# Kernel tuning notes

Hardware: AMD Instinct MI355X
Metric: run time of the kernel (lower is better)

The kernel has to match this reference:

```python
import jax, jax.numpy as jnp
import numpy as np

NUM_USERS = 1_000_000
NUM_MOVIES = 100_000
EMBED_DIM = 64
MLP_SIZES = [16, 8, 4]
BATCH = 16384


def setup_inputs() -> dict:
    key = jax.random.key(0)
    ks = jax.random.split(key, 12)
    s = 0.05
    inp = {
        "user_ids": jax.random.randint(ks[0], (BATCH,), 0, NUM_USERS, dtype=jnp.int32),
        "movie_ids": jax.random.randint(ks[1], (BATCH,), 0, NUM_MOVIES, dtype=jnp.int32),
        "gmf_user_emb": jax.random.normal(ks[2], (NUM_USERS, EMBED_DIM), jnp.float32) * s,
        "gmf_movie_emb": jax.random.normal(ks[3], (NUM_MOVIES, EMBED_DIM), jnp.float32) * s,
        "mlp_user_emb": jax.random.normal(ks[4], (NUM_USERS, MLP_SIZES[0] // 2), jnp.float32) * s,
        "mlp_movie_emb": jax.random.normal(ks[5], (NUM_MOVIES, MLP_SIZES[0] // 2), jnp.float32) * s,
        "W1": jax.random.normal(ks[6], (MLP_SIZES[0], MLP_SIZES[1]), jnp.float32) * s,
        "b1": jnp.zeros((MLP_SIZES[1],), jnp.float32),
        "W2": jax.random.normal(ks[7], (MLP_SIZES[1], MLP_SIZES[2]), jnp.float32) * s,
        "b2": jnp.zeros((MLP_SIZES[2],), jnp.float32),
        "Wf": jax.random.normal(ks[8], (EMBED_DIM + MLP_SIZES[2], 1), jnp.float32) * s,
        "bf": jnp.zeros((1,), jnp.float32),
    }
    return inp


def reference(user_ids, movie_ids, gmf_user_emb, gmf_movie_emb,
              mlp_user_emb, mlp_movie_emb, W1, b1, W2, b2, Wf, bf):
    # GMF branch: elementwise product of gathered embeddings  [B, E]
    gmf_out = gmf_user_emb[user_ids] * gmf_movie_emb[movie_ids]
    # MLP branch: concat gathered halves -> 16 -> 8 -> 4 with ReLU
    mlp_in = jnp.concatenate([mlp_user_emb[user_ids], mlp_movie_emb[movie_ids]], axis=-1)
    h = jax.nn.relu(mlp_in @ W1 + b1)
    h = jax.nn.relu(h @ W2 + b2)
    combined = jnp.concatenate([gmf_out, h], axis=-1)  # [B, E+4]
    logits = combined @ Wf + bf                        # [B, 1]
    out = jax.nn.sigmoid(logits).squeeze(-1) * 4.0 + 1.0
    return out
```

## Files before the change

kernel.cpp:

```cpp
#include <hip/hip_runtime.h>

#define BATCH 16384

__global__ __launch_bounds__(64) void neumf_kernel(
    const int*   __restrict__ user_ids,
    const int*   __restrict__ movie_ids,
    const float* __restrict__ gmf_user,
    const float* __restrict__ gmf_movie,
    const float* __restrict__ mlp_user,
    const float* __restrict__ mlp_movie,
    const float* __restrict__ W1,
    const float* __restrict__ b1,
    const float* __restrict__ W2,
    const float* __restrict__ b2,
    const float* __restrict__ Wf,
    const float* __restrict__ bf,
    float*       __restrict__ out)
{
    int i = blockIdx.x * blockDim.x + threadIdx.x;
    if (i >= BATCH) return;

    const int uid = user_ids[i];
    const int mid = movie_ids[i];

    const float4* u4 = (const float4*)(gmf_user  + (size_t)uid * 64);
    const float4* m4 = (const float4*)(gmf_movie + (size_t)mid * 64);
    const float4* w4 = (const float4*)Wf;

    float acc = 0.f;
    #pragma unroll
    for (int j = 0; j < 16; ++j) {
        float4 a = u4[j];
        float4 b = m4[j];
        float4 w = w4[j];
        acc += a.x * b.x * w.x;
        acc += a.y * b.y * w.y;
        acc += a.z * b.z * w.z;
        acc += a.w * b.w * w.w;
    }

    float in16[16];
    {
        const float4* mu = (const float4*)(mlp_user  + (size_t)uid * 8);
        const float4* mm = (const float4*)(mlp_movie + (size_t)mid * 8);
        float4 t;
        t = mu[0]; in16[0]  = t.x; in16[1]  = t.y; in16[2]  = t.z; in16[3]  = t.w;
        t = mu[1]; in16[4]  = t.x; in16[5]  = t.y; in16[6]  = t.z; in16[7]  = t.w;
        t = mm[0]; in16[8]  = t.x; in16[9]  = t.y; in16[10] = t.z; in16[11] = t.w;
        t = mm[1]; in16[12] = t.x; in16[13] = t.y; in16[14] = t.z; in16[15] = t.w;
    }

    float h1[8];
    #pragma unroll
    for (int j = 0; j < 8; ++j) {
        float s = b1[j];
        #pragma unroll
        for (int k = 0; k < 16; ++k) s = fmaf(in16[k], W1[k * 8 + j], s);
        h1[j] = fmaxf(s, 0.f);
    }

    #pragma unroll
    for (int j = 0; j < 4; ++j) {
        float s = b2[j];
        #pragma unroll
        for (int k = 0; k < 8; ++k) s = fmaf(h1[k], W2[k * 4 + j], s);
        s = fmaxf(s, 0.f);
        acc = fmaf(s, Wf[64 + j], acc);
    }

    const float logit = acc + bf[0];
    const float sig = 1.f / (1.f + __expf(-logit));
    out[i] = sig * 4.f + 1.f;
}

extern "C" void kernel_launch(void* const* d_in, const int* in_sizes, int n_in,
                              void* d_out, int out_size, void* d_ws, size_t ws_size,
                              hipStream_t stream) {
    const int*   user_ids  = (const int*)  d_in[0];
    const int*   movie_ids = (const int*)  d_in[1];
    const float* gmf_user  = (const float*)d_in[2];
    const float* gmf_movie = (const float*)d_in[3];
    const float* mlp_user  = (const float*)d_in[4];
    const float* mlp_movie = (const float*)d_in[5];
    const float* W1        = (const float*)d_in[6];
    const float* b1        = (const float*)d_in[7];
    const float* W2        = (const float*)d_in[8];
    const float* b2        = (const float*)d_in[9];
    const float* Wf        = (const float*)d_in[10];
    const float* bf        = (const float*)d_in[11];
    float*       out       = (float*)d_out;

    const int threads = 64;
    const int blocks  = (BATCH + threads - 1) / threads;
    neumf_kernel<<<blocks, threads, 0, stream>>>(
        user_ids, movie_ids, gmf_user, gmf_movie, mlp_user, mlp_movie,
        W1, b1, W2, b2, Wf, bf, out);
}
```

Before: 9.705 us.

## Split each batch element across 16 lanes with shuffle reduction

Assigns 16 threads per batch element so each lane loads one float4 of the GMF embeddings, which makes the gathered rows coalesced. Partial dot products are combined with xor shuffles. The MLP inputs are loaded by four lanes and broadcast with shuffles. Every lane then computes the small MLP redundantly and lane 0 writes the output. Block size rises to 256. The aim is better memory coalescing and more parallelism for the random gathers, at the cost of redundant MLP arithmetic and shuffle overhead.

```diff
diff --git a/kernel.cpp b/kernel.cpp
--- a/kernel.cpp
+++ b/kernel.cpp
@@ -1,8 +1,9 @@
 #include <hip/hip_runtime.h>
 
 #define BATCH 16384
+#define SPLIT 16
 
-__global__ __launch_bounds__(64) void neumf_kernel(
+__global__ __launch_bounds__(256) void neumf_kernel(
     const int*   __restrict__ user_ids,
     const int*   __restrict__ movie_ids,
     const float* __restrict__ gmf_user,
@@ -17,37 +18,39 @@
     const float* __restrict__ bf,
     float*       __restrict__ out)
 {
-    int i = blockIdx.x * blockDim.x + threadIdx.x;
-    if (i >= BATCH) return;
+    const int tid   = blockIdx.x * blockDim.x + threadIdx.x;
+    const int elem  = tid >> 4;
+    const int lane  = tid & (SPLIT - 1);
+    if (elem >= BATCH) return;
 
-    const int uid = user_ids[i];
-    const int mid = movie_ids[i];
+    const int uid = user_ids[elem];
+    const int mid = movie_ids[elem];
 
-    const float4* u4 = (const float4*)(gmf_user  + (size_t)uid * 64);
-    const float4* m4 = (const float4*)(gmf_movie + (size_t)mid * 64);
-    const float4* w4 = (const float4*)Wf;
+    const float4 u = ((const float4*)(gmf_user  + (size_t)uid * 64))[lane];
+    const float4 m = ((const float4*)(gmf_movie + (size_t)mid * 64))[lane];
+    const float4 w = ((const float4*)Wf)[lane];
 
-    float acc = 0.f;
-    #pragma unroll
-    for (int j = 0; j < 16; ++j) {
-        float4 a = u4[j];
-        float4 b = m4[j];
-        float4 w = w4[j];
-        acc += a.x * b.x * w.x;
-        acc += a.y * b.y * w.y;
-        acc += a.z * b.z * w.z;
-        acc += a.w * b.w * w.w;
-    }
+    float acc = u.x * m.x * w.x;
+    acc = fmaf(u.y * m.y, w.y, acc);
+    acc = fmaf(u.z * m.z, w.z, acc);
+    acc = fmaf(u.w * m.w, w.w, acc);
+
+    acc += __shfl_xor(acc, 1);
+    acc += __shfl_xor(acc, 2);
+    acc += __shfl_xor(acc, 4);
+    acc += __shfl_xor(acc, 8);
+
+    const float* mp = (lane & 2) ? (mlp_movie + (size_t)mid * 8)
+                                 : (mlp_user  + (size_t)uid * 8);
+    const float4 mlpv = ((const float4*)mp)[lane & 1];
 
     float in16[16];
-    {
-        const float4* mu = (const float4*)(mlp_user  + (size_t)uid * 8);
-        const float4* mm = (const float4*)(mlp_movie + (size_t)mid * 8);
-        float4 t;
-        t = mu[0]; in16[0]  = t.x; in16[1]  = t.y; in16[2]  = t.z; in16[3]  = t.w;
-        t = mu[1]; in16[4]  = t.x; in16[5]  = t.y; in16[6]  = t.z; in16[7]  = t.w;
-        t = mm[0]; in16[8]  = t.x; in16[9]  = t.y; in16[10] = t.z; in16[11] = t.w;
-        t = mm[1]; in16[12] = t.x; in16[13] = t.y; in16[14] = t.z; in16[15] = t.w;
+    #pragma unroll
+    for (int c = 0; c < 4; ++c) {
+        in16[c * 4 + 0] = __shfl(mlpv.x, c, SPLIT);
+        in16[c * 4 + 1] = __shfl(mlpv.y, c, SPLIT);
+        in16[c * 4 + 2] = __shfl(mlpv.z, c, SPLIT);
+        in16[c * 4 + 3] = __shfl(mlpv.w, c, SPLIT);
     }
 
     float h1[8];
@@ -59,18 +62,21 @@
         h1[j] = fmaxf(s, 0.f);
     }
 
+    float mlp_acc = 0.f;
     #pragma unroll
     for (int j = 0; j < 4; ++j) {
         float s = b2[j];
         #pragma unroll
         for (int k = 0; k < 8; ++k) s = fmaf(h1[k], W2[k * 4 + j], s);
         s = fmaxf(s, 0.f);
-        acc = fmaf(s, Wf[64 + j], acc);
+        mlp_acc = fmaf(s, Wf[64 + j], mlp_acc);
     }
 
-    const float logit = acc + bf[0];
-    const float sig = 1.f / (1.f + __expf(-logit));
-    out[i] = sig * 4.f + 1.f;
+    if (lane == 0) {
+        const float logit = acc + mlp_acc + bf[0];
+        const float sig = 1.f / (1.f + __expf(-logit));
+        out[elem] = sig * 4.f + 1.f;
+    }
 }
 
 extern "C" void kernel_launch(void* const* d_in, const int* in_sizes, int n_in,
@@ -90,8 +96,9 @@
     const float* bf        = (const float*)d_in[11];
     float*       out       = (float*)d_out;
 
-    const int threads = 64;
-    const int blocks  = (BATCH + threads - 1) / threads;
+    const int threads = 256;
+    const int total   = BATCH * SPLIT;
+    const int blocks  = (total + threads - 1) / threads;
     neumf_kernel<<<blocks, threads, 0, stream>>>(
         user_ids, movie_ids, gmf_user, gmf_movie, mlp_user, mlp_movie,
         W1, b1, W2, b2, Wf, bf, out);
```

Result: no change. 9.756 us (+0.5%).
